# Kernel optimization log

Hardware: AMD Instinct MI355X
Metric: run time of the kernel (lower is better)

## Reference

```python
import jax, jax.numpy as jnp
import numpy as np

H, KVH, D = 32, 8, 128          # heads, kv heads, head dim
WINDOW = 512                     # sliding_window
NEG = -1e30


def _rotate_half(x):
    x1, x2 = jnp.split(x, 2, axis=-1)
    return jnp.concatenate([-x2, x1], axis=-1)


def setup_inputs() -> dict:
    key = jax.random.key(0)
    ks = jax.random.split(key, 6)
    B, S = 4, 1024
    T = B * S
    hidden = H * D  # 4096
    # RoPE tables [max_pos, head_dim]
    inv_freq = 1.0 / (10000.0 ** (jnp.arange(0, D, 2, dtype=jnp.float32) / D))
    freqs = jnp.outer(jnp.arange(S, dtype=jnp.float32), inv_freq)
    emb = jnp.concatenate([freqs, freqs], axis=-1)
    cos, sin = jnp.cos(emb), jnp.sin(emb)
    x = jax.random.normal(ks[0], (T, hidden), dtype=jnp.float32)
    pos = jnp.tile(jnp.arange(S, dtype=jnp.int64), B)            # positions restart per seq
    cu = jnp.arange(B + 1, dtype=jnp.int32) * S                  # uniform varlen offsets
    sc = 0.02
    Wq = jax.random.normal(ks[1], (hidden, H * D), jnp.float32) * sc
    Wk = jax.random.normal(ks[2], (hidden, KVH * D), jnp.float32) * sc
    Wv = jax.random.normal(ks[3], (hidden, KVH * D), jnp.float32) * sc
    Wo = jax.random.normal(ks[4], (H * D, hidden), jnp.float32) * sc
    return {"cos": cos, "sin": sin, "nz_hidden_states": x,
            "nz_position_ids": pos, "cu_seqlens": cu, "max_seqlen": S,
            "Wq": Wq, "Wk": Wk, "Wv": Wv, "Wo": Wo}


def reference(cos, sin, nz_hidden_states, nz_position_ids, cu_seqlens, max_seqlen,
              Wq, Wk, Wv, Wo):
    T = nz_hidden_states.shape[0]
    q = (nz_hidden_states @ Wq).reshape(T, H, D)
    k = (nz_hidden_states @ Wk).reshape(T, KVH, D)
    v = (nz_hidden_states @ Wv).reshape(T, KVH, D)
    # RoPE: gather by position, broadcast over head dim (unsqueeze(-2))
    c = cos[nz_position_ids][:, None, :]
    s = sin[nz_position_ids][:, None, :]
    q = q * c + _rotate_half(q) * s
    k = k * c + _rotate_half(k) * s
    # uniform varlen -> batch view [B, S, ...]
    B = cu_seqlens.shape[0] - 1
    S = T // B
    G = H // KVH  # query heads per kv head (GQA)
    qb = q.reshape(B, S, KVH, G, D)
    kb = k.reshape(B, S, KVH, D)
    vb = v.reshape(B, S, KVH, D)
    scores = jnp.einsum('bqhgd,bkhd->bhgqk', qb, kb) / jnp.sqrt(jnp.float32(D))
    i = jnp.arange(S)[:, None]
    j = jnp.arange(S)[None, :]
    mask = (j <= i) & (i - j <= WINDOW)  # causal + sliding window
    scores = jnp.where(mask, scores, NEG)
    p = jax.nn.softmax(scores, axis=-1)
    out = jnp.einsum('bhgqk,bkhd->bqhgd', p, vb).reshape(T, H * D)
    return out @ Wo
```

## Files before the change

kernel.cpp:

```cpp
#include <hip/hip_runtime.h>

typedef __bf16 bf16_t;
typedef __bf16 bf16x8 __attribute__((ext_vector_type(8)));
typedef __bf16 bf16x4 __attribute__((ext_vector_type(4)));
typedef float  f32x4  __attribute__((ext_vector_type(4)));
typedef float  f32x16 __attribute__((ext_vector_type(16)));
typedef unsigned int u32x4 __attribute__((ext_vector_type(4)));

#define N_HEADS 32
#define N_KVH   8
#define HEADDIM 128
#define WINDOW  512
#define NBATCH  4
#define SEQLEN  1024
#define NTOK    (NBATCH * SEQLEN)
#define HIDDEN  4096
#define QKVW    6144

__device__ __forceinline__ void llds16(const bf16_t* g, const bf16_t* l)
{
    __builtin_amdgcn_global_load_lds(
        (const __attribute__((address_space(1))) void*)g,
        (__attribute__((address_space(3))) void*)l, 16, 0, 0);
}

template<bool OUT_F32>
__global__ __launch_bounds__(512, 2)
void gemm256_kernel(const bf16_t* __restrict__ A, const bf16_t* __restrict__ Bt,
                    void* __restrict__ Cp, int M, int N, int K)
{
    __shared__ __align__(16) char lds[4 * 32768];
    const int tid  = threadIdx.x;
    const int w    = tid >> 6, lane = tid & 63;
    const int ntx  = N >> 8;
    const int nwg  = gridDim.x;
    const int cpx  = nwg >> 3;
    const int lin  = blockIdx.x;
    const int swz  = (nwg & 7) == 0 ? (lin & 7) * cpx + (lin >> 3) : lin;
    const int m0   = (swz / ntx) * 256;
    const int n0   = (swz % ntx) * 256;
    const int wm   = (w >> 2) * 128;
    const int wn   = (w & 3) * 64;
    const int fr   = lane & 15;
    const int kslot16 = (((lane >> 4) ^ ((lane >> 1) & 3)) << 4);
    const int srcblk  = (((tid & 3) ^ ((tid >> 3) & 3)) << 3);
    const int nk = K >> 5;

    f32x4 acc[8][4];
#pragma unroll
    for (int i = 0; i < 8; ++i)
#pragma unroll
        for (int j = 0; j < 4; ++j) {
            acc[i][j][0] = 0.f; acc[i][j][1] = 0.f;
            acc[i][j][2] = 0.f; acc[i][j][3] = 0.f;
        }

    const bf16_t* arow = A  + (size_t)(m0 + (tid >> 2)) * K + srcblk;
    const bf16_t* brow = Bt + (size_t)(n0 + (tid >> 2)) * K + srcblk;
    const size_t rowK128 = (size_t)128 * K;

    auto STAGE = [&](int tt) {
        char* dst = lds + (tt & 3) * 32768 + w * 1024;
        const int kt = tt << 5;
#pragma unroll
        for (int j = 0; j < 2; ++j)
            llds16(arow + j * rowK128 + kt, (const bf16_t*)(dst + j * 8192));
#pragma unroll
        for (int j = 0; j < 2; ++j)
            llds16(brow + j * rowK128 + kt, (const bf16_t*)(dst + 16384 + j * 8192));
    };

    STAGE(0); STAGE(1); STAGE(2);

    for (int t = 0; t < nk; ++t) {
        if (t < nk - 2)       asm volatile("s_waitcnt vmcnt(8)" ::: "memory");
        else if (t == nk - 2) asm volatile("s_waitcnt vmcnt(4)" ::: "memory");
        else                  asm volatile("s_waitcnt vmcnt(0)" ::: "memory");
        __builtin_amdgcn_sched_barrier(0);
        __builtin_amdgcn_s_barrier();
        __builtin_amdgcn_sched_barrier(0);

        const char* base = lds + (t & 3) * 32768;
        bf16x8 af[8], bfg[4];
#pragma unroll
        for (int mt = 0; mt < 8; ++mt)
            af[mt] = *(const bf16x8*)(base + ((wm + mt * 16 + fr) << 6) + kslot16);
#pragma unroll
        for (int nt = 0; nt < 4; ++nt)
            bfg[nt] = *(const bf16x8*)(base + 16384 + ((wn + nt * 16 + fr) << 6) + kslot16);

        if (t + 3 < nk) STAGE(t + 3);
        __builtin_amdgcn_s_setprio(1);
#pragma unroll
        for (int mt = 0; mt < 8; ++mt)
#pragma unroll
            for (int nt = 0; nt < 4; ++nt)
                acc[mt][nt] = __builtin_amdgcn_mfma_f32_16x16x32_bf16(
                    af[mt], bfg[nt], acc[mt][nt], 0, 0, 0);
        __builtin_amdgcn_s_setprio(0);
    }

    const int r0 = (lane >> 4) << 2;
#pragma unroll
    for (int mt = 0; mt < 8; ++mt)
#pragma unroll
        for (int nt = 0; nt < 4; ++nt)
#pragma unroll
            for (int r = 0; r < 4; ++r) {
                int row = m0 + wm + mt * 16 + r0 + r;
                int col = n0 + wn + nt * 16 + fr;
                if constexpr (OUT_F32)
                    ((float*)Cp)[(size_t)row * N + col] = acc[mt][nt][r];
                else
                    ((bf16_t*)Cp)[(size_t)row * N + col] = (bf16_t)acc[mt][nt][r];
            }
}

template<bool A_F32, bool OUT_F32>
__global__ __launch_bounds__(256)
void gemm_kernel(const void* __restrict__ Ap, const void* __restrict__ Bp,
                 void* __restrict__ Cp, int M, int N, int K)
{
    __shared__ bf16_t As[128 * 40];
    __shared__ bf16_t Bs[128 * 40];
    const int tid  = threadIdx.x;
    const int m0   = blockIdx.y * 128;
    const int n0   = blockIdx.x * 128;
    const int wave = tid >> 6, lane = tid & 63;
    const int wm   = (wave >> 1) * 64, wn = (wave & 1) * 64;
    const int fr   = lane & 15;
    const int koff = (lane >> 4) * 8;

    f32x4 acc[4][4];
#pragma unroll
    for (int i = 0; i < 4; ++i)
#pragma unroll
        for (int j = 0; j < 4; ++j) {
            acc[i][j][0] = 0.f; acc[i][j][1] = 0.f;
            acc[i][j][2] = 0.f; acc[i][j][3] = 0.f;
        }

    for (int kt = 0; kt < K; kt += 32) {
        __syncthreads();
        if constexpr (A_F32) {
            const float* A = (const float*)Ap;
#pragma unroll
            for (int i = 0; i < 4; ++i) {
                int lin = tid + i * 256;
                int row = lin >> 3;
                int kq  = (lin & 7) << 2;
                const float4 v = *(const float4*)(A + (size_t)(m0 + row) * K + kt + kq);
                bf16_t* d = &As[row * 40 + kq];
                d[0] = (bf16_t)v.x; d[1] = (bf16_t)v.y;
                d[2] = (bf16_t)v.z; d[3] = (bf16_t)v.w;
            }
        } else {
            const bf16_t* A = (const bf16_t*)Ap;
#pragma unroll
            for (int i = 0; i < 2; ++i) {
                int lin = tid + i * 256;
                int row = lin >> 2;
                int kq  = (lin & 3) << 3;
                *(bf16x8*)&As[row * 40 + kq] =
                    *(const bf16x8*)(A + (size_t)(m0 + row) * K + kt + kq);
            }
        }
        {
            const float* B = (const float*)Bp;
#pragma unroll
            for (int i = 0; i < 4; ++i) {
                int lin = tid + i * 256;
                int kr  = lin >> 5;
                int nc  = (lin & 31) << 2;
                const float4 v = *(const float4*)(B + (size_t)(kt + kr) * N + n0 + nc);
                Bs[(nc + 0) * 40 + kr] = (bf16_t)v.x;
                Bs[(nc + 1) * 40 + kr] = (bf16_t)v.y;
                Bs[(nc + 2) * 40 + kr] = (bf16_t)v.z;
                Bs[(nc + 3) * 40 + kr] = (bf16_t)v.w;
            }
        }
        __syncthreads();
        bf16x8 af[4], bfg[4];
#pragma unroll
        for (int mt = 0; mt < 4; ++mt)
            af[mt] = *(const bf16x8*)&As[(wm + mt * 16 + fr) * 40 + koff];
#pragma unroll
        for (int nt = 0; nt < 4; ++nt)
            bfg[nt] = *(const bf16x8*)&Bs[(wn + nt * 16 + fr) * 40 + koff];
#pragma unroll
        for (int mt = 0; mt < 4; ++mt)
#pragma unroll
            for (int nt = 0; nt < 4; ++nt)
                acc[mt][nt] = __builtin_amdgcn_mfma_f32_16x16x32_bf16(
                    af[mt], bfg[nt], acc[mt][nt], 0, 0, 0);
    }
    const int r0 = (lane >> 4) << 2;
#pragma unroll
    for (int mt = 0; mt < 4; ++mt)
#pragma unroll
        for (int nt = 0; nt < 4; ++nt)
#pragma unroll
            for (int r = 0; r < 4; ++r) {
                int row = m0 + wm + mt * 16 + r0 + r;
                int col = n0 + wn + nt * 16 + fr;
                if constexpr (OUT_F32)
                    ((float*)Cp)[(size_t)row * N + col] = acc[mt][nt][r];
                else
                    ((bf16_t*)Cp)[(size_t)row * N + col] = (bf16_t)acc[mt][nt][r];
            }
}

__global__ __launch_bounds__(256)
void f32_to_bf16_kernel(const float* __restrict__ in, bf16_t* __restrict__ out, int n8)
{
    int i = blockIdx.x * 256 + threadIdx.x;
    if (i >= n8) return;
    const float4 a = *(const float4*)(in + (size_t)i * 8);
    const float4 b = *(const float4*)(in + (size_t)i * 8 + 4);
    bf16x8 v;
    v[0] = (bf16_t)a.x; v[1] = (bf16_t)a.y; v[2] = (bf16_t)a.z; v[3] = (bf16_t)a.w;
    v[4] = (bf16_t)b.x; v[5] = (bf16_t)b.y; v[6] = (bf16_t)b.z; v[7] = (bf16_t)b.w;
    *(bf16x8*)(out + (size_t)i * 8) = v;
}

__global__ __launch_bounds__(256)
void wtrans_kernel(const float* __restrict__ W, bf16_t* __restrict__ Wt, int K, int N)
{
    __shared__ bf16_t tile[32][33];
    const int k0 = blockIdx.x * 32;
    const int n0 = blockIdx.y * 32;
    const int c  = threadIdx.x & 31, r0 = threadIdx.x >> 5;
#pragma unroll
    for (int i = 0; i < 4; ++i) {
        int r = r0 + i * 8;
        tile[r][c] = (bf16_t)W[(size_t)(k0 + r) * N + n0 + c];
    }
    __syncthreads();
#pragma unroll
    for (int i = 0; i < 4; ++i) {
        int r = r0 + i * 8;
        Wt[(size_t)(n0 + r) * K + k0 + c] = tile[c][r];
    }
}

__global__ __launch_bounds__(256)
void rope_kernel(bf16_t* __restrict__ qb, int qstr, bf16_t* __restrict__ kb, int kstr,
                 const float* __restrict__ cosT, const float* __restrict__ sinT)
{
    int lin  = blockIdx.x * 256 + threadIdx.x;
    int d    = lin & 63;
    int rest = lin >> 6;
    int head = rest % (N_HEADS + N_KVH);
    int t    = rest / (N_HEADS + N_KVH);
    if (t >= NTOK) return;
    int p = t & (SEQLEN - 1);
    float c = cosT[p * HEADDIM + d];
    float s = sinT[p * HEADDIM + d];
    bf16_t* ptr;
    float sc;
    if (head < N_HEADS) { ptr = qb + (size_t)t * qstr + head * HEADDIM; sc = 0.08838834764831845f; }
    else                { ptr = kb + (size_t)t * kstr + (head - N_HEADS) * HEADDIM; sc = 1.0f; }
    float x1 = (float)ptr[d], x2 = (float)ptr[d + 64];
    ptr[d]      = (bf16_t)((x1 * c - x2 * s) * sc);
    ptr[d + 64] = (bf16_t)((x2 * c + x1 * s) * sc);
}

__global__ __launch_bounds__(256)
void vtrans_kernel(const bf16_t* __restrict__ Vs, int vstr, bf16_t* __restrict__ Vt)
{
    __shared__ bf16_t tile[32][33];
    const int s0  = blockIdx.x * 32;
    const int d0  = blockIdx.y * 32;
    const int bk  = blockIdx.z;
    const int b   = bk >> 3, kvh = bk & 7;
    const int c   = threadIdx.x & 31, r0 = threadIdx.x >> 5;
    const bf16_t* src = Vs + (size_t)(b * SEQLEN + s0) * vstr + kvh * HEADDIM + d0;
#pragma unroll
    for (int i = 0; i < 4; ++i) {
        int r = r0 + i * 8;
        tile[r][c] = src[(size_t)r * vstr + c];
    }
    __syncthreads();
    bf16_t* dst = Vt + ((size_t)(b * N_KVH + kvh) * HEADDIM + d0) * SEQLEN + s0;
#pragma unroll
    for (int i = 0; i < 4; ++i) {
        int dr = r0 + i * 8;
        dst[(size_t)dr * SEQLEN + c] = tile[c][dr];
    }
}

__device__ __forceinline__ unsigned int pk2(float a, float b)
{
    unsigned short x = __builtin_bit_cast(unsigned short, (bf16_t)a);
    unsigned short y = __builtin_bit_cast(unsigned short, (bf16_t)b);
    return ((unsigned int)y << 16) | (unsigned int)x;
}
__device__ __forceinline__ void swap32(unsigned int& a, unsigned int& b)
{
    asm volatile("v_permlane32_swap_b32 %0, %1" : "+v"(a), "+v"(b));
}

__device__ __forceinline__ void stage_kv(const bf16_t* __restrict__ Kb, int kstr,
                                         const bf16_t* __restrict__ Vt,
                                         char* ldsb, int bb, int kvh, int kb,
                                         int w, int i)
{
#pragma unroll
    for (int j = 0; j < 2; ++j) {
        int row = w * 8 + j * 4 + (i >> 4);
        const bf16_t* src = Kb + (size_t)(bb * SEQLEN + kb + row) * kstr + kvh * HEADDIM
                          + (((i & 15) ^ (row & 7)) << 3);
        llds16(src, (const bf16_t*)(ldsb + (w * 8 + j * 4) * 256));
    }
#pragma unroll
    for (int j = 0; j < 2; ++j) {
        int d = w * 16 + j * 8 + (i >> 3);
        const bf16_t* src = Vt + ((size_t)((bb * N_KVH + kvh) * HEADDIM + d)) * SEQLEN + kb
                          + (((i & 7) ^ (d & 7)) << 3);
        llds16(src, (const bf16_t*)(ldsb + 16384 + (w * 16 + j * 8) * 128));
    }
}

__global__ __launch_bounds__(512, 2)
void attn32_kernel(const bf16_t* __restrict__ Qb, const bf16_t* __restrict__ Kb,
                   const bf16_t* __restrict__ Vt, bf16_t* __restrict__ Ob,
                   int qstr, int kstr)
{
    __shared__ __align__(16) char lds[65536];
    const int tid = threadIdx.x, w = tid >> 6, i = tid & 63;
    const int la = i & 31, hi = i >> 5;
    const int qt = blockIdx.x, kvh = blockIdx.y, bb = blockIdx.z;
    const int Q0 = qt * 64;
    const int h  = kvh * 4 + (w >> 1);
    const int qw = Q0 + 32 * (w & 1);
    const int KL = Q0 >= WINDOW ? Q0 - WINDOW : 0;
    const int nt = (Q0 - KL) / 64 + 1;
    const int iq = qw + la;

    const bf16_t* qp = Qb + (size_t)(bb * SEQLEN + iq) * qstr + h * HEADDIM + 8 * hi;
    bf16x8 qf[8];
#pragma unroll
    for (int c = 0; c < 8; ++c) qf[c] = *(const bf16x8*)(qp + c * 16);

    f32x16 oacc[4];
#pragma unroll
    for (int d = 0; d < 4; ++d)
#pragma unroll
        for (int r = 0; r < 16; ++r) oacc[d][r] = 0.f;
    float mrow = -1e30f, lsum = 0.f;

    stage_kv(Kb, kstr, Vt, lds, bb, kvh, KL, w, i);

    const int cswz = (la & 7) << 4;

    for (int t = 0; t < nt; ++t) {
        asm volatile("s_waitcnt vmcnt(0) lgkmcnt(0)" ::: "memory");
        __builtin_amdgcn_sched_barrier(0);
        __syncthreads();
        if (t + 1 < nt)
            stage_kv(Kb, kstr, Vt, lds + ((t + 1) & 1) * 32768, bb, kvh, KL + (t + 1) * 64, w, i);
        const char* KsB = lds + (t & 1) * 32768;
        const char* VsB = KsB + 16384;
        const int kb = KL + t * 64;

        f32x16 s0, s1;
#pragma unroll
        for (int r = 0; r < 16; ++r) { s0[r] = 0.f; s1[r] = 0.f; }
        __builtin_amdgcn_s_setprio(1);
#pragma unroll
        for (int c = 0; c < 8; ++c) {
            bf16x8 k0 = *(const bf16x8*)(KsB + la * 256        + ((c * 32 + 16 * hi) ^ cswz));
            bf16x8 k1 = *(const bf16x8*)(KsB + (la + 32) * 256 + ((c * 32 + 16 * hi) ^ cswz));
            s0 = __builtin_amdgcn_mfma_f32_32x32x16_bf16(k0, qf[c], s0, 0, 0, 0);
            s1 = __builtin_amdgcn_mfma_f32_32x32x16_bf16(k1, qf[c], s1, 0, 0, 0);
        }
        __builtin_amdgcn_s_setprio(0);

        const bool interior = (kb + 63 <= qw) && (kb >= qw - (WINDOW - 31));
        if (!interior) {
#pragma unroll
            for (int r = 0; r < 16; ++r) {
                int j0 = kb + (r & 3) + 8 * (r >> 2) + 4 * hi;
                int j1 = j0 + 32;
                if (!(j0 <= iq && iq - j0 <= WINDOW)) s0[r] = -1e30f;
                if (!(j1 <= iq && iq - j1 <= WINDOW)) s1[r] = -1e30f;
            }
        }

        float mt = fmaxf(s0[0], s1[0]);
#pragma unroll
        for (int r = 1; r < 16; ++r) mt = fmaxf(mt, fmaxf(s0[r], s1[r]));
        mt = fmaxf(mt, __shfl_xor(mt, 32, 64));
        float mnew = fmaxf(mrow, mt);
        float corr = __expf(mrow - mnew);
        float ps = 0.f;
#pragma unroll
        for (int r = 0; r < 16; ++r) {
            s0[r] = __expf(s0[r] - mnew);
            s1[r] = __expf(s1[r] - mnew);
            ps += s0[r] + s1[r];
        }
        ps += __shfl_xor(ps, 32, 64);
        lsum = lsum * corr + ps;
        mrow = mnew;
#pragma unroll
        for (int d = 0; d < 4; ++d)
#pragma unroll
            for (int r = 0; r < 16; ++r) oacc[d][r] *= corr;

        bf16x8 pa[4];
        {
            unsigned int w0 = pk2(s0[0], s0[1]),  w1 = pk2(s0[2], s0[3]);
            unsigned int w2 = pk2(s0[4], s0[5]),  w3 = pk2(s0[6], s0[7]);
            swap32(w0, w2); swap32(w1, w3);
            u32x4 u; u[0] = w0; u[1] = w1; u[2] = w2; u[3] = w3;
            pa[0] = __builtin_bit_cast(bf16x8, u);
            w0 = pk2(s0[8], s0[9]);   w1 = pk2(s0[10], s0[11]);
            w2 = pk2(s0[12], s0[13]); w3 = pk2(s0[14], s0[15]);
            swap32(w0, w2); swap32(w1, w3);
            u[0] = w0; u[1] = w1; u[2] = w2; u[3] = w3;
            pa[1] = __builtin_bit_cast(bf16x8, u);
            w0 = pk2(s1[0], s1[1]);  w1 = pk2(s1[2], s1[3]);
            w2 = pk2(s1[4], s1[5]);  w3 = pk2(s1[6], s1[7]);
            swap32(w0, w2); swap32(w1, w3);
            u[0] = w0; u[1] = w1; u[2] = w2; u[3] = w3;
            pa[2] = __builtin_bit_cast(bf16x8, u);
            w0 = pk2(s1[8], s1[9]);   w1 = pk2(s1[10], s1[11]);
            w2 = pk2(s1[12], s1[13]); w3 = pk2(s1[14], s1[15]);
            swap32(w0, w2); swap32(w1, w3);
            u[0] = w0; u[1] = w1; u[2] = w2; u[3] = w3;
            pa[3] = __builtin_bit_cast(bf16x8, u);
        }

        __builtin_amdgcn_s_setprio(1);
#pragma unroll
        for (int d = 0; d < 4; ++d) {
            const char* vrow = VsB + (d * 32 + la) * 128;
#pragma unroll
            for (int ks = 0; ks < 4; ++ks) {
                bf16x8 vf = *(const bf16x8*)(vrow + ((ks * 32 + 16 * hi) ^ cswz));
                oacc[d] = __builtin_amdgcn_mfma_f32_32x32x16_bf16(vf, pa[ks], oacc[d], 0, 0, 0);
            }
        }
        __builtin_amdgcn_s_setprio(0);
    }

    float rn = 1.f / lsum;
    bf16_t* orow = Ob + ((size_t)((bb * SEQLEN + iq) * N_HEADS + h)) * HEADDIM;
#pragma unroll
    for (int d = 0; d < 4; ++d)
#pragma unroll
        for (int g = 0; g < 4; ++g) {
            bf16x4 v;
            v[0] = (bf16_t)(oacc[d][4 * g + 0] * rn);
            v[1] = (bf16_t)(oacc[d][4 * g + 1] * rn);
            v[2] = (bf16_t)(oacc[d][4 * g + 2] * rn);
            v[3] = (bf16_t)(oacc[d][4 * g + 3] * rn);
            *(bf16x4*)(orow + d * 32 + 8 * g + 4 * hi) = v;
        }
}

extern "C" void kernel_launch(void* const* d_in, const int* in_sizes, int n_in,
                              void* d_out, int out_size, void* d_ws, size_t ws_size,
                              hipStream_t stream)
{
    const float* cosT = (const float*)d_in[0];
    const float* sinT = (const float*)d_in[1];
    const float* x    = (const float*)d_in[2];
    const float* Wq   = (const float*)d_in[6];
    const float* Wk   = (const float*)d_in[7];
    const float* Wv   = (const float*)d_in[8];
    const float* Wo   = (const float*)d_in[9];
    float* out = (float*)d_out;
    char* ws = (char*)d_ws;
    const size_t MB = 1024ull * 1024ull;

    if (ws_size >= 136 * MB) {
        bf16_t* Xb    = (bf16_t*)(ws);
        bf16_t* Wqkvt = (bf16_t*)(ws + 32 * MB);
        bf16_t* QKVb  = (bf16_t*)(ws + 80 * MB);
        bf16_t* Vt    = (bf16_t*)(ws + 128 * MB);
        bf16_t* Ob    = Xb;

        f32_to_bf16_kernel<<<(NTOK * HIDDEN / 8 + 255) / 256, 256, 0, stream>>>(x, Xb, NTOK * HIDDEN / 8);
        wtrans_kernel<<<dim3(HIDDEN/32, HIDDEN/32), 256, 0, stream>>>(Wq, Wqkvt, HIDDEN, HIDDEN);
        wtrans_kernel<<<dim3(HIDDEN/32, 1024/32), 256, 0, stream>>>(Wk, Wqkvt + (size_t)4096 * HIDDEN, HIDDEN, 1024);
        wtrans_kernel<<<dim3(HIDDEN/32, 1024/32), 256, 0, stream>>>(Wv, Wqkvt + (size_t)5120 * HIDDEN, HIDDEN, 1024);
        gemm256_kernel<false><<<dim3((NTOK/256) * (QKVW/256)), 512, 0, stream>>>(Xb, Wqkvt, QKVb, NTOK, QKVW, HIDDEN);
        rope_kernel<<<(NTOK * (N_HEADS + N_KVH) * 64) / 256, 256, 0, stream>>>(QKVb, QKVW, QKVb + 4096, QKVW, cosT, sinT);
        vtrans_kernel<<<dim3(SEQLEN/32, HEADDIM/32, NBATCH * N_KVH), 256, 0, stream>>>(QKVb + 5120, QKVW, Vt);
        attn32_kernel<<<dim3(SEQLEN/64, N_KVH, NBATCH), 512, 0, stream>>>(QKVb, QKVb + 4096, Vt, Ob, QKVW, QKVW);
        wtrans_kernel<<<dim3(HIDDEN/32, HIDDEN/32), 256, 0, stream>>>(Wo, Wqkvt, HIDDEN, HIDDEN);
        gemm256_kernel<true><<<dim3((NTOK/256) * (HIDDEN/256)), 512, 0, stream>>>(Ob, Wqkvt, out, NTOK, HIDDEN, HIDDEN);
    } else {
        bf16_t* Qb = (bf16_t*)(ws);
        bf16_t* Kb = (bf16_t*)(ws + 32 * MB);
        bf16_t* Vb = (bf16_t*)(ws + 40 * MB);
        bf16_t* Vt = (bf16_t*)(ws + 48 * MB);
        bf16_t* Ob = (bf16_t*)(ws + 56 * MB);
        gemm_kernel<true, false><<<dim3(32, 32), 256, 0, stream>>>(x, Wq, Qb, NTOK, HIDDEN, HIDDEN);
        gemm_kernel<true, false><<<dim3(8, 32), 256, 0, stream>>>(x, Wk, Kb, NTOK, 1024, HIDDEN);
        gemm_kernel<true, false><<<dim3(8, 32), 256, 0, stream>>>(x, Wv, Vb, NTOK, 1024, HIDDEN);
        rope_kernel<<<(NTOK * (N_HEADS + N_KVH) * 64) / 256, 256, 0, stream>>>(Qb, HIDDEN, Kb, 1024, cosT, sinT);
        vtrans_kernel<<<dim3(SEQLEN/32, HEADDIM/32, NBATCH * N_KVH), 256, 0, stream>>>(Vb, 1024, Vt);
        attn32_kernel<<<dim3(SEQLEN/64, N_KVH, NBATCH), 512, 0, stream>>>(Qb, Kb, Vt, Ob, HIDDEN, 1024);
        gemm_kernel<false, true><<<dim3(32, 32), 256, 0, stream>>>(Ob, Wo, out, NTOK, HIDDEN, HIDDEN);
    }
}
```

Baseline: 504.9 us.

## Fuse prep kernels, move Q RoPE into attention, retile GEMM to 256x128

Merges the input cast and all weight transposes into one prep kernel, and merges K RoPE with the V transpose into one kernel. Q RoPE and the softmax scale now run inside the attention kernel on the loaded Q fragments, so Q is no longer rewritten in memory. The GEMM is retiled from 256x256 to 256x128 with a 3-stage LDS ring and 4 blocks per CU, giving more workgroups and higher occupancy but less reuse per block. Together these cut launch count and memory passes, at the cost of a larger prep grid and more attention prologue work.

```diff
diff --git a/kernel.cpp b/kernel.cpp
--- a/kernel.cpp
+++ b/kernel.cpp
@@ -25,30 +25,30 @@
 }
 
 template<bool OUT_F32>
-__global__ __launch_bounds__(512, 2)
-void gemm256_kernel(const bf16_t* __restrict__ A, const bf16_t* __restrict__ Bt,
-                    void* __restrict__ Cp, int M, int N, int K)
-{
-    __shared__ __align__(16) char lds[4 * 32768];
+__global__ __launch_bounds__(512, 4)
+void gemm_dual_kernel(const bf16_t* __restrict__ A, const bf16_t* __restrict__ Bt,
+                      void* __restrict__ Cp, int M, int N, int K)
+{
+    __shared__ __align__(16) char lds[3 * 24576];
     const int tid  = threadIdx.x;
     const int w    = tid >> 6, lane = tid & 63;
-    const int ntx  = N >> 8;
+    const int ntx  = N >> 7;
     const int nwg  = gridDim.x;
     const int cpx  = nwg >> 3;
     const int lin  = blockIdx.x;
     const int swz  = (nwg & 7) == 0 ? (lin & 7) * cpx + (lin >> 3) : lin;
     const int m0   = (swz / ntx) * 256;
-    const int n0   = (swz % ntx) * 256;
-    const int wm   = (w >> 2) * 128;
-    const int wn   = (w & 3) * 64;
+    const int n0   = (swz % ntx) * 128;
+    const int wm   = (w >> 1) * 64;
+    const int wn   = (w & 1) * 64;
     const int fr   = lane & 15;
     const int kslot16 = (((lane >> 4) ^ ((lane >> 1) & 3)) << 4);
     const int srcblk  = (((tid & 3) ^ ((tid >> 3) & 3)) << 3);
     const int nk = K >> 5;
 
-    f32x4 acc[8][4];
-#pragma unroll
-    for (int i = 0; i < 8; ++i)
+    f32x4 acc[4][4];
+#pragma unroll
+    for (int i = 0; i < 4; ++i)
 #pragma unroll
         for (int j = 0; j < 4; ++j) {
             acc[i][j][0] = 0.f; acc[i][j][1] = 0.f;
@@ -59,50 +59,51 @@
     const bf16_t* brow = Bt + (size_t)(n0 + (tid >> 2)) * K + srcblk;
     const size_t rowK128 = (size_t)128 * K;
 
-    auto STAGE = [&](int tt) {
-        char* dst = lds + (tt & 3) * 32768 + w * 1024;
+    auto STAGE = [&](int tt, int buf) {
+        char* dst = lds + buf * 24576 + w * 1024;
         const int kt = tt << 5;
-#pragma unroll
-        for (int j = 0; j < 2; ++j)
-            llds16(arow + j * rowK128 + kt, (const bf16_t*)(dst + j * 8192));
-#pragma unroll
-        for (int j = 0; j < 2; ++j)
-            llds16(brow + j * rowK128 + kt, (const bf16_t*)(dst + 16384 + j * 8192));
+        llds16(arow + kt,           (const bf16_t*)(dst));
+        llds16(arow + rowK128 + kt, (const bf16_t*)(dst + 8192));
+        llds16(brow + kt,           (const bf16_t*)(dst + 16384));
     };
 
-    STAGE(0); STAGE(1); STAGE(2);
-
+    STAGE(0, 0); STAGE(1, 1);
+
+    int cur = 0;
     for (int t = 0; t < nk; ++t) {
-        if (t < nk - 2)       asm volatile("s_waitcnt vmcnt(8)" ::: "memory");
-        else if (t == nk - 2) asm volatile("s_waitcnt vmcnt(4)" ::: "memory");
-        else                  asm volatile("s_waitcnt vmcnt(0)" ::: "memory");
+        if (t + 1 < nk) asm volatile("s_waitcnt vmcnt(3)" ::: "memory");
+        else            asm volatile("s_waitcnt vmcnt(0)" ::: "memory");
         __builtin_amdgcn_sched_barrier(0);
         __builtin_amdgcn_s_barrier();
         __builtin_amdgcn_sched_barrier(0);
 
-        const char* base = lds + (t & 3) * 32768;
-        bf16x8 af[8], bfg[4];
-#pragma unroll
-        for (int mt = 0; mt < 8; ++mt)
+        const char* base = lds + cur * 24576;
+        bf16x8 af[4], bfg[4];
+#pragma unroll
+        for (int mt = 0; mt < 4; ++mt)
             af[mt] = *(const bf16x8*)(base + ((wm + mt * 16 + fr) << 6) + kslot16);
 #pragma unroll
         for (int nt = 0; nt < 4; ++nt)
             bfg[nt] = *(const bf16x8*)(base + 16384 + ((wn + nt * 16 + fr) << 6) + kslot16);
 
-        if (t + 3 < nk) STAGE(t + 3);
+        if (t + 2 < nk) {
+            int nb = cur + 2; if (nb >= 3) nb -= 3;
+            STAGE(t + 2, nb);
+        }
         __builtin_amdgcn_s_setprio(1);
 #pragma unroll
-        for (int mt = 0; mt < 8; ++mt)
+        for (int mt = 0; mt < 4; ++mt)
 #pragma unroll
             for (int nt = 0; nt < 4; ++nt)
                 acc[mt][nt] = __builtin_amdgcn_mfma_f32_16x16x32_bf16(
                     af[mt], bfg[nt], acc[mt][nt], 0, 0, 0);
         __builtin_amdgcn_s_setprio(0);
+        ++cur; if (cur == 3) cur = 0;
     }
 
     const int r0 = (lane >> 4) << 2;
 #pragma unroll
-    for (int mt = 0; mt < 8; ++mt)
+    for (int mt = 0; mt < 4; ++mt)
 #pragma unroll
         for (int nt = 0; nt < 4; ++nt)
 #pragma unroll
@@ -211,16 +212,44 @@
 }
 
 __global__ __launch_bounds__(256)
-void f32_to_bf16_kernel(const float* __restrict__ in, bf16_t* __restrict__ out, int n8)
-{
-    int i = blockIdx.x * 256 + threadIdx.x;
-    if (i >= n8) return;
-    const float4 a = *(const float4*)(in + (size_t)i * 8);
-    const float4 b = *(const float4*)(in + (size_t)i * 8 + 4);
-    bf16x8 v;
-    v[0] = (bf16_t)a.x; v[1] = (bf16_t)a.y; v[2] = (bf16_t)a.z; v[3] = (bf16_t)a.w;
-    v[4] = (bf16_t)b.x; v[5] = (bf16_t)b.y; v[6] = (bf16_t)b.z; v[7] = (bf16_t)b.w;
-    *(bf16x8*)(out + (size_t)i * 8) = v;
+void prep_kernel(const float* __restrict__ x,
+                 const float* __restrict__ Wq, const float* __restrict__ Wk,
+                 const float* __restrict__ Wv, const float* __restrict__ Wo,
+                 bf16_t* __restrict__ Xb, bf16_t* __restrict__ Wqkvt,
+                 bf16_t* __restrict__ WoT)
+{
+    __shared__ bf16_t tile[32][33];
+    const int bid = blockIdx.x;
+    if (bid < 8192) {
+        int i = bid * 256 + threadIdx.x;
+        const float4 a = *(const float4*)(x + (size_t)i * 8);
+        const float4 b = *(const float4*)(x + (size_t)i * 8 + 4);
+        bf16x8 v;
+        v[0] = (bf16_t)a.x; v[1] = (bf16_t)a.y; v[2] = (bf16_t)a.z; v[3] = (bf16_t)a.w;
+        v[4] = (bf16_t)b.x; v[5] = (bf16_t)b.y; v[6] = (bf16_t)b.z; v[7] = (bf16_t)b.w;
+        *(bf16x8*)(Xb + (size_t)i * 8) = v;
+        return;
+    }
+    const float* W; bf16_t* Wt; int j;
+    if (bid < 24576)      { W = Wq; Wt = Wqkvt;                          j = bid - 8192; }
+    else if (bid < 28672) { W = Wk; Wt = Wqkvt + (size_t)4096 * HIDDEN;  j = bid - 24576; }
+    else if (bid < 32768) { W = Wv; Wt = Wqkvt + (size_t)5120 * HIDDEN;  j = bid - 28672; }
+    else                  { W = Wo; Wt = WoT;                            j = bid - 32768; }
+    const int N  = (bid >= 24576 && bid < 32768) ? 1024 : HIDDEN;
+    const int k0 = (j & 127) << 5;
+    const int n0 = (j >> 7) << 5;
+    const int c  = threadIdx.x & 31, r0 = threadIdx.x >> 5;
+#pragma unroll
+    for (int i = 0; i < 4; ++i) {
+        int r = r0 + i * 8;
+        tile[r][c] = (bf16_t)W[(size_t)(k0 + r) * N + n0 + c];
+    }
+    __syncthreads();
+#pragma unroll
+    for (int i = 0; i < 4; ++i) {
+        int r = r0 + i * 8;
+        Wt[(size_t)(n0 + r) * HIDDEN + k0 + c] = tile[c][r];
+    }
 }
 
 __global__ __launch_bounds__(256)
@@ -244,34 +273,32 @@
 }
 
 __global__ __launch_bounds__(256)
-void rope_kernel(bf16_t* __restrict__ qb, int qstr, bf16_t* __restrict__ kb, int kstr,
-                 const float* __restrict__ cosT, const float* __restrict__ sinT)
-{
-    int lin  = blockIdx.x * 256 + threadIdx.x;
-    int d    = lin & 63;
-    int rest = lin >> 6;
-    int head = rest % (N_HEADS + N_KVH);
-    int t    = rest / (N_HEADS + N_KVH);
-    if (t >= NTOK) return;
-    int p = t & (SEQLEN - 1);
-    float c = cosT[p * HEADDIM + d];
-    float s = sinT[p * HEADDIM + d];
-    bf16_t* ptr;
-    float sc;
-    if (head < N_HEADS) { ptr = qb + (size_t)t * qstr + head * HEADDIM; sc = 0.08838834764831845f; }
-    else                { ptr = kb + (size_t)t * kstr + (head - N_HEADS) * HEADDIM; sc = 1.0f; }
-    float x1 = (float)ptr[d], x2 = (float)ptr[d + 64];
-    ptr[d]      = (bf16_t)((x1 * c - x2 * s) * sc);
-    ptr[d + 64] = (bf16_t)((x2 * c + x1 * s) * sc);
-}
-
-__global__ __launch_bounds__(256)
-void vtrans_kernel(const bf16_t* __restrict__ Vs, int vstr, bf16_t* __restrict__ Vt)
+void ropek_vtrans_kernel(bf16_t* __restrict__ kb, int kstr,
+                         const bf16_t* __restrict__ Vs, int vstr,
+                         bf16_t* __restrict__ Vt,
+                         const float* __restrict__ cosT, const float* __restrict__ sinT)
 {
     __shared__ bf16_t tile[32][33];
-    const int s0  = blockIdx.x * 32;
-    const int d0  = blockIdx.y * 32;
-    const int bk  = blockIdx.z;
+    const int bid = blockIdx.x;
+    if (bid < 8192) {
+        int lin  = bid * 256 + threadIdx.x;
+        int d    = lin & 63;
+        int rest = lin >> 6;
+        int kvh  = rest & 7;
+        int t    = rest >> 3;
+        int p    = t & (SEQLEN - 1);
+        float c = cosT[p * HEADDIM + d];
+        float s = sinT[p * HEADDIM + d];
+        bf16_t* ptr = kb + (size_t)t * kstr + kvh * HEADDIM;
+        float x1 = (float)ptr[d], x2 = (float)ptr[d + 64];
+        ptr[d]      = (bf16_t)(x1 * c - x2 * s);
+        ptr[d + 64] = (bf16_t)(x2 * c + x1 * s);
+        return;
+    }
+    int j = bid - 8192;
+    const int s0  = (j & 31) * 32;
+    const int d0  = ((j >> 5) & 3) * 32;
+    const int bk  = j >> 7;
     const int b   = bk >> 3, kvh = bk & 7;
     const int c   = threadIdx.x & 31, r0 = threadIdx.x >> 5;
     const bf16_t* src = Vs + (size_t)(b * SEQLEN + s0) * vstr + kvh * HEADDIM + d0;
@@ -324,7 +351,8 @@
 __global__ __launch_bounds__(512, 2)
 void attn32_kernel(const bf16_t* __restrict__ Qb, const bf16_t* __restrict__ Kb,
                    const bf16_t* __restrict__ Vt, bf16_t* __restrict__ Ob,
-                   int qstr, int kstr)
+                   int qstr, int kstr,
+                   const float* __restrict__ cosT, const float* __restrict__ sinT)
 {
     __shared__ __align__(16) char lds[65536];
     const int tid = threadIdx.x, w = tid >> 6, i = tid & 63;
@@ -341,6 +369,27 @@
     bf16x8 qf[8];
 #pragma unroll
     for (int c = 0; c < 8; ++c) qf[c] = *(const bf16x8*)(qp + c * 16);
+
+    {
+        const float sc = 0.08838834764831845f;
+        const float* crow = cosT + (size_t)iq * HEADDIM + 8 * hi;
+        const float* srow = sinT + (size_t)iq * HEADDIM + 8 * hi;
+#pragma unroll
+        for (int c = 0; c < 4; ++c) {
+            float4 c0 = *(const float4*)(crow + c * 16);
+            float4 c1 = *(const float4*)(crow + c * 16 + 4);
+            float4 sA = *(const float4*)(srow + c * 16);
+            float4 sB = *(const float4*)(srow + c * 16 + 4);
+            float cc[8] = {c0.x, c0.y, c0.z, c0.w, c1.x, c1.y, c1.z, c1.w};
+            float ss[8] = {sA.x, sA.y, sA.z, sA.w, sB.x, sB.y, sB.z, sB.w};
+#pragma unroll
+            for (int j = 0; j < 8; ++j) {
+                float x1 = (float)qf[c][j], x2 = (float)qf[c + 4][j];
+                qf[c][j]     = (bf16_t)((x1 * cc[j] - x2 * ss[j]) * sc);
+                qf[c + 4][j] = (bf16_t)((x2 * cc[j] + x1 * ss[j]) * sc);
+            }
+        }
+    }
 
     f32x16 oacc[4];
 #pragma unroll
@@ -481,17 +530,17 @@
         bf16_t* QKVb  = (bf16_t*)(ws + 80 * MB);
         bf16_t* Vt    = (bf16_t*)(ws + 128 * MB);
         bf16_t* Ob    = Xb;
-
-        f32_to_bf16_kernel<<<(NTOK * HIDDEN / 8 + 255) / 256, 256, 0, stream>>>(x, Xb, NTOK * HIDDEN / 8);
-        wtrans_kernel<<<dim3(HIDDEN/32, HIDDEN/32), 256, 0, stream>>>(Wq, Wqkvt, HIDDEN, HIDDEN);
-        wtrans_kernel<<<dim3(HIDDEN/32, 1024/32), 256, 0, stream>>>(Wk, Wqkvt + (size_t)4096 * HIDDEN, HIDDEN, 1024);
-        wtrans_kernel<<<dim3(HIDDEN/32, 1024/32), 256, 0, stream>>>(Wv, Wqkvt + (size_t)5120 * HIDDEN, HIDDEN, 1024);
-        gemm256_kernel<false><<<dim3((NTOK/256) * (QKVW/256)), 512, 0, stream>>>(Xb, Wqkvt, QKVb, NTOK, QKVW, HIDDEN);
-        rope_kernel<<<(NTOK * (N_HEADS + N_KVH) * 64) / 256, 256, 0, stream>>>(QKVb, QKVW, QKVb + 4096, QKVW, cosT, sinT);
-        vtrans_kernel<<<dim3(SEQLEN/32, HEADDIM/32, NBATCH * N_KVH), 256, 0, stream>>>(QKVb + 5120, QKVW, Vt);
-        attn32_kernel<<<dim3(SEQLEN/64, N_KVH, NBATCH), 512, 0, stream>>>(QKVb, QKVb + 4096, Vt, Ob, QKVW, QKVW);
-        wtrans_kernel<<<dim3(HIDDEN/32, HIDDEN/32), 256, 0, stream>>>(Wo, Wqkvt, HIDDEN, HIDDEN);
-        gemm256_kernel<true><<<dim3((NTOK/256) * (HIDDEN/256)), 512, 0, stream>>>(Ob, Wqkvt, out, NTOK, HIDDEN, HIDDEN);
+        const bool withWo = ws_size >= 168 * MB;
+        bf16_t* WoT = withWo ? (bf16_t*)(ws + 136 * MB) : Wqkvt;
+
+        const int prep_blocks = 8192 + 16384 + 4096 + 4096 + (withWo ? 16384 : 0);
+        prep_kernel<<<prep_blocks, 256, 0, stream>>>(x, Wq, Wk, Wv, Wo, Xb, Wqkvt, WoT);
+        gemm_dual_kernel<false><<<dim3((NTOK/256) * (QKVW/128)), 512, 0, stream>>>(Xb, Wqkvt, QKVb, NTOK, QKVW, HIDDEN);
+        if (!withWo)
+            wtrans_kernel<<<dim3(HIDDEN/32, HIDDEN/32), 256, 0, stream>>>(Wo, Wqkvt, HIDDEN, HIDDEN);
+        ropek_vtrans_kernel<<<8192 + 4096, 256, 0, stream>>>(QKVb + 4096, QKVW, QKVb + 5120, QKVW, Vt, cosT, sinT);
+        attn32_kernel<<<dim3(SEQLEN/64, N_KVH, NBATCH), 512, 0, stream>>>(QKVb, QKVb + 4096, Vt, Ob, QKVW, QKVW, cosT, sinT);
+        gemm_dual_kernel<true><<<dim3((NTOK/256) * (HIDDEN/128)), 512, 0, stream>>>(Ob, WoT, out, NTOK, HIDDEN, HIDDEN);
     } else {
         bf16_t* Qb = (bf16_t*)(ws);
         bf16_t* Kb = (bf16_t*)(ws + 32 * MB);
@@ -501,9 +550,8 @@
         gemm_kernel<true, false><<<dim3(32, 32), 256, 0, stream>>>(x, Wq, Qb, NTOK, HIDDEN, HIDDEN);
         gemm_kernel<true, false><<<dim3(8, 32), 256, 0, stream>>>(x, Wk, Kb, NTOK, 1024, HIDDEN);
         gemm_kernel<true, false><<<dim3(8, 32), 256, 0, stream>>>(x, Wv, Vb, NTOK, 1024, HIDDEN);
-        rope_kernel<<<(NTOK * (N_HEADS + N_KVH) * 64) / 256, 256, 0, stream>>>(Qb, HIDDEN, Kb, 1024, cosT, sinT);
-        vtrans_kernel<<<dim3(SEQLEN/32, HEADDIM/32, NBATCH * N_KVH), 256, 0, stream>>>(Vb, 1024, Vt);
-        attn32_kernel<<<dim3(SEQLEN/64, N_KVH, NBATCH), 512, 0, stream>>>(Qb, Kb, Vt, Ob, HIDDEN, 1024);
+        ropek_vtrans_kernel<<<8192 + 4096, 256, 0, stream>>>(Kb, 1024, Vb, 1024, Vt, cosT, sinT);
+        attn32_kernel<<<dim3(SEQLEN/64, N_KVH, NBATCH), 512, 0, stream>>>(Qb, Kb, Vt, Ob, HIDDEN, 1024, cosT, sinT);
         gemm_kernel<false, true><<<dim3(32, 32), 256, 0, stream>>>(Ob, Wo, out, NTOK, HIDDEN, HIDDEN);
     }
 }
```

Result: no change. 502.8 us (-0.4%).
